# Optimization experiments

Measured on AMD Instinct MI355X. Metric: run time of the kernel, lower is better.

The kernel has to match this reference:

```python
import jax, jax.numpy as jnp
import numpy as np

# Irreps config: node = 64x0e + 32x1o, edge sh = 1x0e + 1x1o
N, E = 50000, 800000
MUL0, MUL1 = 64, 32
D_IN = MUL0 + 3 * MUL1          # 160
FC_H = 64
W_NUMEL = MUL0 + MUL0 + MUL1 + MUL1  # 192, per-instruction uvu weights
SQRT3 = 1.7320508075688772
ACT_C = 1.6791   # e3nn normalize2mom constant for silu


def setup_inputs() -> dict:
    key = jax.random.key(0)
    ks = jax.random.split(key, 11)
    return {
        "x": jax.random.normal(ks[0], (N, D_IN), jnp.float32),
        "edge_scalars": jax.random.uniform(ks[1], (E, FC_H), dtype=jnp.float32),
        "edge_attr_sh": jax.random.normal(ks[2], (E, 4), jnp.float32),
        "edge_index": jax.random.randint(ks[3], (2, E), 0, N),
        "w_fc1": jax.random.normal(ks[4], (FC_H, FC_H), jnp.float32),
        "w_fc2": jax.random.normal(ks[5], (FC_H, W_NUMEL), jnp.float32),
        "w_sc_s": jax.random.normal(ks[6], (MUL0, MUL0), jnp.float32),
        "w_sc_v": jax.random.normal(ks[7], (MUL1, MUL1), jnp.float32),
        "w_lin_s": jax.random.normal(ks[8], (96, MUL0), jnp.float32),
        "w_lin_v": jax.random.normal(ks[9], (96, MUL1), jnp.float32),
        "w_alpha": jax.random.normal(ks[10], (96, 1), jnp.float32) * 0.1,
    }


def reference(x, edge_scalars, edge_attr_sh, edge_index, w_fc1, w_fc2,
              w_sc_s, w_sc_v, w_lin_s, w_lin_v, w_alpha):
    src, dst = edge_index[0], edge_index[1]

    # --- fc: FullyConnectedNet([64, 64, 192], silu), e3nn fan-in norm ---
    h = jax.nn.silu(edge_scalars @ w_fc1 / np.sqrt(FC_H)) * ACT_C
    weight = h @ w_fc2 / np.sqrt(FC_H)                       # [E, 192]
    w0 = weight[:, :MUL0]                 # 0e x 0e -> 0e (mul 64)
    w1 = weight[:, MUL0:2 * MUL0]         # 0e x 1o -> 1o (mul 64)
    w2 = weight[:, 2 * MUL0:2 * MUL0 + MUL1]   # 1o x 0e -> 1o (mul 32)
    w3 = weight[:, 2 * MUL0 + MUL1:]           # 1o x 1o -> 0e (mul 32)

    # --- self connection: o3.Linear(in -> out), per-irrep mixing ---
    x_s = x[:, :MUL0]                                   # [N, 64]
    x_v = x[:, MUL0:].reshape(N, MUL1, 3)               # [N, 32, 3]
    sc_s = x_s @ w_sc_s / np.sqrt(MUL0)
    sc_v = jnp.einsum('nui,uw->nwi', x_v, w_sc_v) / np.sqrt(MUL1)
    sc_out = jnp.concatenate([sc_s, sc_v.reshape(N, 3 * MUL1)], axis=1)

    # --- gather + edge-weighted uvu tensor product ---
    gx_s = x_s[src]                                     # [E, 64]
    gx_v = x_v[src]                                     # [E, 32, 3]
    sh_s = edge_attr_sh[:, 0:1]                         # [E, 1]
    sh_v = edge_attr_sh[:, 1:4]                         # [E, 3]

    # path weights fold with w3j so factors cancel for 1o outputs
    mid_s0 = w0 * gx_s * sh_s                                        # [E,64] 0e
    mid_s1 = w3 * jnp.einsum('eui,ei->eu', gx_v, sh_v) / SQRT3       # [E,32] 0e
    mid_v0 = w1[:, :, None] * gx_s[:, :, None] * sh_v[:, None, :]    # [E,64,3] 1o
    mid_v1 = w2[:, :, None] * gx_v * sh_s[:, :, None]                # [E,32,3] 1o
    edge_feat = jnp.concatenate(
        [mid_s0, mid_s1, mid_v0.reshape(E, 3 * MUL0), mid_v1.reshape(E, 3 * MUL1)],
        axis=1)                                                      # [E, 384]

    # --- scatter-mean to destination nodes ---
    seg = jax.ops.segment_sum(edge_feat, dst, num_segments=N)
    cnt = jax.ops.segment_sum(jnp.ones((E,), edge_feat.dtype), dst, num_segments=N)
    mean = seg / jnp.maximum(cnt, 1.0)[:, None]                      # [N, 384]

    m_s = mean[:, :96]                                   # 96x0e
    m_v = mean[:, 96:].reshape(N, 96, 3)                 # 96x1o

    # --- alpha gate (o3.Linear mid -> 0e) and output linear ---
    alpha = m_s @ w_alpha / np.sqrt(96)                  # [N, 1]
    lin_s = m_s @ w_lin_s / np.sqrt(96)                  # [N, 64]
    lin_v = jnp.einsum('nui,uw->nwi', m_v, w_lin_v) / np.sqrt(96)
    lin_out = jnp.concatenate([lin_s, lin_v.reshape(N, 3 * MUL1)], axis=1)

    # sc.output_mask is all-ones here (every output irrep reachable)
    return sc_out + alpha * lin_out
```

## Files before the change

kernel.cpp:

```cpp
#include <hip/hip_runtime.h>
#include <hip/hip_bf16.h>

#define N_NODES 50000
#define N_EDGES 800000
#define MUL0 64
#define MUL1 32
#define D_IN 160
#define FC_H 64
#define W_NUMEL 192
#define FEAT 384
#define ACT_C 1.6791f
#define INV_SQRT3 0.57735026918962576f
#define RSQRT32 0.17677669529663687f
#define RSQRT96 0.10206207261596575f

#define TILE 64

typedef __attribute__((ext_vector_type(8))) short s16x8;
typedef __attribute__((ext_vector_type(4))) float f32x4;
typedef _Float16 h8 __attribute__((ext_vector_type(8)));
typedef __fp16 fp16x2 __attribute__((ext_vector_type(2)));

static __device__ __forceinline__ unsigned short f2bf(float f) {
    __hip_bfloat16 b = __float2bfloat16(f);
    return __builtin_bit_cast(unsigned short, b);
}

static __device__ __forceinline__ int swz(int row, int byte_in_row) {
    int unit = ((row & 1) << 2) | (byte_in_row >> 4);
    int su = unit ^ ((row >> 1) & 7);
    return (row >> 1) * 128 + su * 16 + (byte_in_row & 15);
}
static __device__ __forceinline__ h8 rdh8(const unsigned char* base, int row, int eb) {
    return *(const h8*)(base + swz(row, eb));
}


__global__ __launch_bounds__(256) void hist_kernel(const int* __restrict__ eidx,
                                                   int* __restrict__ cnt) {
    int e = blockIdx.x * 256 + threadIdx.x;
    if (e < N_EDGES) atomicAdd(&cnt[eidx[N_EDGES + e]], 1);
}

#define SCAN_NB 64
#define SCAN_CH ((N_NODES + SCAN_NB - 1) / SCAN_NB)

__global__ __launch_bounds__(256) void scanA_kernel(const int* __restrict__ cnt,
                                                    int* __restrict__ bsum) {
    __shared__ int sred[4];
    int b = blockIdx.x, t = threadIdx.x;
    int lim = min((b + 1) * SCAN_CH, N_NODES);
    int s = 0;
    for (int i = b * SCAN_CH + t; i < lim; i += 256) s += cnt[i];
    for (int d = 1; d < 64; d <<= 1) s += __shfl_xor(s, d);
    if ((t & 63) == 0) sred[t >> 6] = s;
    __syncthreads();
    if (t == 0) bsum[b] = sred[0] + sred[1] + sred[2] + sred[3];
}

__global__ __launch_bounds__(64) void scanB_kernel(const int* __restrict__ bsum,
                                                   int* __restrict__ boff) {
    int t = threadIdx.x;
    int v = bsum[t];
    int p = v;
    for (int d = 1; d < 64; d <<= 1) { int u = __shfl_up(p, d); if (t >= d) p += u; }
    boff[t] = p - v;
}

__global__ __launch_bounds__(256) void scanC_kernel(const int* __restrict__ cnt,
                                                    const int* __restrict__ boff,
                                                    int* __restrict__ fill) {
    __shared__ int s_w[4];
    int b = blockIdx.x, t = threadIdx.x;
    const int CH2 = (SCAN_CH + 255) / 256;
    int base = b * SCAN_CH + t * CH2;
    int lim = min((b + 1) * SCAN_CH, N_NODES);
    int s = 0;
#pragma unroll
    for (int k = 0; k < CH2; ++k) { int i = base + k; if (i < lim) s += cnt[i]; }
    int v = s;
    for (int d = 1; d < 64; d <<= 1) { int u = __shfl_up(v, d); if ((t & 63) >= d) v += u; }
    if ((t & 63) == 63) s_w[t >> 6] = v;
    __syncthreads();
    if (t == 0) { int run = 0; for (int w = 0; w < 4; ++w) { int tv = s_w[w]; s_w[w] = run; run += tv; } }
    __syncthreads();
    int run = boff[b] + s_w[t >> 6] + (v - s);
#pragma unroll
    for (int k = 0; k < CH2; ++k) {
        int i = base + k;
        if (i < lim) { fill[i] = run; run += cnt[i]; }
    }
}

__global__ __launch_bounds__(256) void scatter_ids_kernel(const int* __restrict__ eidx,
                                                          int* __restrict__ fill,
                                                          int* __restrict__ sorted_eid) {
    int e = blockIdx.x * 256 + threadIdx.x;
    if (e < N_EDGES) {
        int p = atomicAdd(&fill[eidx[N_EDGES + e]], 1);
        sorted_eid[p] = e;
    }
}

__global__ __launch_bounds__(256) void prep_w_kernel(
    const float* __restrict__ w_fc1,
    const float* __restrict__ w_fc2,
    const float* __restrict__ w_sc_s,
    const float* __restrict__ w_sc_v,
    const float* __restrict__ w_lin_s,
    const float* __restrict__ w_lin_v,
    unsigned short* __restrict__ w1t,
    unsigned short* __restrict__ w2t,
    unsigned short* __restrict__ wscs_t,
    unsigned short* __restrict__ wscv_t,
    unsigned short* __restrict__ wlins_t,
    unsigned short* __restrict__ wlinv_t)
{
    int i = blockIdx.x * 256 + threadIdx.x;
    if (i < 64 * 64)  w1t[i]    = f2bf(w_fc1[(i & 63) * FC_H + (i >> 6)]);
    if (i < 192 * 64) w2t[i]    = f2bf(w_fc2[(i & 63) * W_NUMEL + (i >> 6)]);
    if (i < 64 * 64)  wscs_t[i] = f2bf(w_sc_s[(i & 63) * 64 + (i >> 6)]);
    if (i < 32 * 32)  wscv_t[i] = f2bf(w_sc_v[(i & 31) * 32 + (i >> 5)]);
    if (i < 64 * 96)  wlins_t[i] = f2bf(w_lin_s[(i % 96) * 64 + (i / 96)]);
    if (i < 32 * 96)  wlinv_t[i] = f2bf(w_lin_v[(i % 96) * 32 + (i / 96)]);
}

#define X_OFF    0
#define W_OFF    20480
#define SH_OFF   45056
#define SID_OFF  45568
#define SEGN_OFF 45696
#define NSEG_OFF 45952
#define SMEM_SZ  45968

static __device__ __forceinline__ h8 seg_mask(const unsigned* vv, unsigned tgt) {
    h8 a;
#pragma unroll
    for (int w2 = 0; w2 < 4; ++w2) {
        a[w2 * 2]     = ((vv[w2] & 0xffffu) == tgt) ? (_Float16)1.f : (_Float16)0.f;
        a[w2 * 2 + 1] = ((vv[w2] >> 16)     == tgt) ? (_Float16)1.f : (_Float16)0.f;
    }
    return a;
}

__global__ __launch_bounds__(256) void edge_kernel(
    const float* __restrict__ x,
    const float* __restrict__ es,
    const float* __restrict__ sh,
    const int*   __restrict__ eidx,
    const int*   __restrict__ sorted_eid,
    const unsigned short* __restrict__ w1t,
    const unsigned short* __restrict__ w2t,
    float* __restrict__ accg)
{
    __shared__ __align__(16) unsigned char smem[SMEM_SZ];
    int* s_segnode = (int*)(smem + SEGN_OFF);
    unsigned short* s_sid = (unsigned short*)(smem + SID_OFF);

    const int t = threadIdx.x;
    const int l = t & 63;
    const int wv = t >> 6;
    const int lr = l & 15;
    const int lk = l >> 4;
    const int tile0 = blockIdx.x * TILE;

    int eid_own = sorted_eid[tile0 + wv * 16 + lr];
    float4 esf[4];
    {
        const float4* ep = (const float4*)(es + (size_t)eid_own * FC_H);
        esf[0] = ep[lk * 2];     esf[1] = ep[lk * 2 + 1];
        esf[2] = ep[8 + lk * 2]; esf[3] = ep[8 + lk * 2 + 1];
    }
    const int hs   = t >> 7;
    const int tt_h = t & 127;
    const int xe   = tt_h & 31;
    const int cgrp = tt_h >> 5;
    float4 xg[10];
    {
        const float4* xp = (const float4*)(x + (size_t)eidx[sorted_eid[tile0 + hs * 32 + xe]] * D_IN);
#pragma unroll
        for (int k = 0; k < 10; ++k) xg[k] = xp[cgrp * 10 + k];
    }
    float shv = sh[(size_t)sorted_eid[tile0 + (t >> 2)] * 4 + (t & 3)];
    if (wv == 0) {
        int dl = eidx[N_EDGES + sorted_eid[tile0 + l]];
        int nd = __shfl_down(dl, 1);
        bool flag = (l == 63) || (dl != nd);
        unsigned long long m = __ballot(flag);
        int sid = __popcll(m & ((1ull << l) - 1ull));
        s_sid[l] = (unsigned short)sid;
        if (flag) s_segnode[sid] = dl;
        if (l == 63) *(int*)(smem + NSEG_OFF) = sid + 1;
    }

    unsigned short* s_h = (unsigned short*)(smem + X_OFF);
    s16x8 afrag[2];
    {
        s16x8 a;
        a[0] = f2bf(esf[0].x); a[1] = f2bf(esf[0].y); a[2] = f2bf(esf[0].z); a[3] = f2bf(esf[0].w);
        a[4] = f2bf(esf[1].x); a[5] = f2bf(esf[1].y); a[6] = f2bf(esf[1].z); a[7] = f2bf(esf[1].w);
        afrag[0] = a;
        a[0] = f2bf(esf[2].x); a[1] = f2bf(esf[2].y); a[2] = f2bf(esf[2].z); a[3] = f2bf(esf[2].w);
        a[4] = f2bf(esf[3].x); a[5] = f2bf(esf[3].y); a[6] = f2bf(esf[3].z); a[7] = f2bf(esf[3].w);
        afrag[1] = a;
    }
#pragma unroll
    for (int nt = 0; nt < 4; ++nt) {
        f32x4 hacc = {0.f, 0.f, 0.f, 0.f};
#pragma unroll
        for (int kk = 0; kk < 2; ++kk) {
            s16x8 b = *(const s16x8*)(w1t + (nt * 16 + lr) * 64 + kk * 32 + lk * 8);
            hacc = __builtin_amdgcn_mfma_f32_16x16x32_bf16(afrag[kk], b, hacc, 0, 0, 0);
        }
#pragma unroll
        for (int q = 0; q < 4; ++q) {
            float aa = hacc[q] * 0.125f;
            float hv = aa * (1.f / (1.f + __expf(-aa))) * ACT_C;
            s_h[(wv * 16 + lk * 4 + q) * 72 + nt * 16 + lr] = f2bf(hv);
        }
    }
    s16x8 hfrag[2];
#pragma unroll
    for (int kk = 0; kk < 2; ++kk)
        hfrag[kk] = *(const s16x8*)(s_h + (wv * 16 + lr) * 72 + kk * 32 + lk * 8);
    __syncthreads();

    {
        const int ws = wv >> 1;
        const int ebyte = (wv & 1) * 32 + lk * 8;
        unsigned char* bw = smem + W_OFF + ws * 12288;
#pragma unroll
        for (int nt = 0; nt < 12; ++nt) {
            f32x4 acc = {0.f, 0.f, 0.f, 0.f};
#pragma unroll
            for (int kk = 0; kk < 2; ++kk) {
                s16x8 b = *(const s16x8*)(w2t + (nt * 16 + lr) * 64 + kk * 32 + lk * 8);
                acc = __builtin_amdgcn_mfma_f32_16x16x32_bf16(hfrag[kk], b, acc, 0, 0, 0);
            }
            int f = nt * 16 + lr;
            fp16x2 p0 = __builtin_amdgcn_cvt_pkrtz(acc[0] * 0.125f, acc[1] * 0.125f);
            fp16x2 p1 = __builtin_amdgcn_cvt_pkrtz(acc[2] * 0.125f, acc[3] * 0.125f);
            uint2 wval = { __builtin_bit_cast(unsigned, p0), __builtin_bit_cast(unsigned, p1) };
            *(uint2*)(bw + swz(f, ebyte)) = wval;
        }
    }
    {
        unsigned char* bx = smem + X_OFF + hs * 10240;
#pragma unroll
        for (int k = 0; k < 10; ++k) {
            float4 v = xg[k];
#pragma unroll
            for (int jj = 0; jj < 4; ++jj) {
                int r = (cgrp * 10 + k) * 4 + jj;
                float fv = (jj == 0) ? v.x : (jj == 1) ? v.y : (jj == 2) ? v.z : v.w;
                *(_Float16*)(bx + swz(r, xe * 2)) = (_Float16)fv;
            }
        }
    }
    {
        int e = t >> 2, c = t & 3;
        *(_Float16*)(smem + SH_OFF + (e >> 5) * 256 + swz(c, (e & 31) * 2)) = (_Float16)shv;
    }
    __syncthreads();

    const int nseg = *(const int*)(smem + NSEG_OFF);
    const int eb = lk * 16;

    h8 shreg[4][2];
    unsigned vv[2][4];
#pragma unroll
    for (int ks = 0; ks < 2; ++ks) {
#pragma unroll
        for (int r = 0; r < 4; ++r)
            shreg[r][ks] = rdh8(smem + SH_OFF + ks * 256, r, eb);
        uint4 sv = *(const uint4*)(smem + SID_OFF + ks * 64 + lk * 16);
        vv[ks][0] = sv.x; vv[ks][1] = sv.y; vv[ks][2] = sv.z; vv[ks][3] = sv.w;
    }

    h8 Bv[4][2];
    int fcol[4];
    bool cls3j[4] = {false, false, false, false};
#pragma unroll
    for (int ks = 0; ks < 2; ++ks) {
        const unsigned char* bx = smem + X_OFF + ks * 10240;
        const unsigned char* bw = smem + W_OFF + ks * 12288;
        if (wv == 0) {
#pragma unroll
            for (int jj = 0; jj < 4; ++jj) {
                int col = jj * 16 + lr;
                Bv[jj][ks] = rdh8(bw, col, eb) * rdh8(bx, col, eb);
                fcol[jj] = col;
            }
        } else if (wv == 1) {
#pragma unroll
            for (int jj = 0; jj < 4; ++jj) {
                int col = jj * 16 + lr;
                Bv[jj][ks] = rdh8(bw, 128 + col / 3, eb) * rdh8(bx, 64 + col, eb);
                fcol[jj] = 288 + col;
            }
        } else if (wv == 2) {
#pragma unroll
            for (int jj = 0; jj < 2; ++jj) {
                int col = 64 + jj * 16 + lr;
                Bv[jj][ks] = rdh8(bw, 128 + col / 3, eb) * rdh8(bx, 64 + col, eb);
                fcol[jj] = 288 + col;
            }
#pragma unroll
            for (int jj = 2; jj < 4; ++jj) {
                int col = (jj - 2) * 16 + lr;
                h8 d = rdh8(bx, 64 + 3 * col, eb)     * shreg[1][ks]
                     + rdh8(bx, 64 + 3 * col + 1, eb) * shreg[2][ks]
                     + rdh8(bx, 64 + 3 * col + 2, eb) * shreg[3][ks];
                Bv[jj][ks] = rdh8(bw, 160 + col, eb) * d;
                fcol[jj] = 64 + col;
                cls3j[jj] = true;
            }
        } else {
#pragma unroll
            for (int jj = 0; jj < 4; ++jj) {
                int col = jj * 16 + lr;
                Bv[jj][ks] = rdh8(bw, 64 + col, eb) * rdh8(bx, col, eb);
                fcol[jj] = 96 + 3 * col;
            }
        }
    }

    if (wv != 3) {
        const int npass = (nseg + 15) >> 4;
        for (int p = 0; p < npass; ++p) {
            h8 bm0 = seg_mask(vv[0], (unsigned)(p * 16 + lr));
            h8 bm1 = seg_mask(vv[1], (unsigned)(p * 16 + lr));
            h8 As0 = bm0 * shreg[0][0];
            h8 As1 = bm1 * shreg[0][1];
            const int m0 = p * 16 + lk * 4;
            float* nptr[4]; bool valid[4], atq[4];
#pragma unroll
            for (int q = 0; q < 4; ++q) {
                int sg = m0 + q;
                valid[q] = sg < nseg;
                int node = valid[q] ? s_segnode[sg] : 0;
                nptr[q] = accg + (size_t)node * FEAT;
                atq[q] = (sg == 0) || (sg == nseg - 1);
            }
#pragma unroll
            for (int jj = 0; jj < 4; ++jj) {
                f32x4 acc = {0.f, 0.f, 0.f, 0.f};
                acc = __builtin_amdgcn_mfma_f32_16x16x32_f16(cls3j[jj] ? bm0 : As0, Bv[jj][0], acc, 0, 0, 0);
                acc = __builtin_amdgcn_mfma_f32_16x16x32_f16(cls3j[jj] ? bm1 : As1, Bv[jj][1], acc, 0, 0, 0);
                const float sc = cls3j[jj] ? INV_SQRT3 : 1.f;
#pragma unroll
                for (int q = 0; q < 4; ++q) {
                    if (valid[q]) {
                        float v = acc[q] * sc;
                        float* a = nptr[q] + fcol[jj];
                        if (atq[q]) atomicAdd(a, v); else *a = v;
                    }
                }
            }
        }
    } else {
        const int npass = (3 * nseg + 15) >> 4;
        for (int p = 0; p < npass; ++p) {
            int m = p * 16 + lr;
            int sgA = m / 3, i3A = m - 3 * sgA;
            h8 mk0 = seg_mask(vv[0], (unsigned)sgA);
            h8 mk1 = seg_mask(vv[1], (unsigned)sgA);
            h8 A0 = mk0 * ((i3A == 0) ? shreg[1][0] : (i3A == 1) ? shreg[2][0] : shreg[3][0]);
            h8 A1 = mk1 * ((i3A == 0) ? shreg[1][1] : (i3A == 1) ? shreg[2][1] : shreg[3][1]);
            int m0 = p * 16 + lk * 4;
            int sgq = m0 / 3, rq = m0 - 3 * sgq;
            float* nptr[4]; int i3q[4]; bool valid[4], atq[4];
#pragma unroll
            for (int q = 0; q < 4; ++q) {
                valid[q] = sgq < nseg;
                int node = valid[q] ? s_segnode[sgq] : 0;
                nptr[q] = accg + (size_t)node * FEAT;
                i3q[q] = rq;
                atq[q] = (sgq == 0) || (sgq == nseg - 1);
                if (++rq == 3) { rq = 0; ++sgq; }
            }
#pragma unroll
            for (int jj = 0; jj < 4; ++jj) {
                f32x4 acc = {0.f, 0.f, 0.f, 0.f};
                acc = __builtin_amdgcn_mfma_f32_16x16x32_f16(A0, Bv[jj][0], acc, 0, 0, 0);
                acc = __builtin_amdgcn_mfma_f32_16x16x32_f16(A1, Bv[jj][1], acc, 0, 0, 0);
#pragma unroll
                for (int q = 0; q < 4; ++q) {
                    if (valid[q]) {
                        float* a = nptr[q] + fcol[jj] + i3q[q];
                        if (atq[q]) atomicAdd(a, acc[q]); else *a = acc[q];
                    }
                }
            }
        }
    }
}


static __device__ __forceinline__ s16x8 frag_c8(const float* p, float s) {
    float4 u = *(const float4*)p, v = *(const float4*)(p + 4);
    s16x8 a;
    a[0] = f2bf(u.x * s); a[1] = f2bf(u.y * s); a[2] = f2bf(u.z * s); a[3] = f2bf(u.w * s);
    a[4] = f2bf(v.x * s); a[5] = f2bf(v.y * s); a[6] = f2bf(v.z * s); a[7] = f2bf(v.w * s);
    return a;
}

__global__ __launch_bounds__(256) void node_kernel(
    const float* __restrict__ x,
    const float* __restrict__ accg,
    const int*   __restrict__ cnt,
    const unsigned short* __restrict__ wscs_t,
    const unsigned short* __restrict__ wscv_t,
    const unsigned short* __restrict__ wlins_t,
    const unsigned short* __restrict__ wlinv_t,
    const float* __restrict__ w_alpha,
    float* __restrict__ out)
{
    const int t = threadIdx.x;
    const int wv = t >> 6, l = t & 63;
    const int lr = l & 15, lk = l >> 4;
    const int n_base = blockIdx.x * 64 + wv * 16;
    const int nrow = n_base + lr;
    const int nclamp = min(nrow, N_NODES - 1);

    const float* mrow = accg + (size_t)nclamp * FEAT;
    const float* xrow = x + (size_t)nclamp * D_IN;
    const float rinv = 1.f / (float)max(cnt[nclamp], 1);

    s16x8 ax[2], ams[3], axv[3], amv[3][3];
#pragma unroll
    for (int kk = 0; kk < 2; ++kk) ax[kk] = frag_c8(xrow + kk * 32 + lk * 8, 1.f);
#pragma unroll
    for (int kk = 0; kk < 3; ++kk) ams[kk] = frag_c8(mrow + kk * 32 + lk * 8, rinv);
    {
        float xb[24];
        const float4* p = (const float4*)(xrow + 64 + 24 * lk);
#pragma unroll
        for (int q = 0; q < 6; ++q) ((float4*)xb)[q] = p[q];
#pragma unroll
        for (int i = 0; i < 3; ++i) {
            s16x8 a;
#pragma unroll
            for (int j = 0; j < 8; ++j) a[j] = f2bf(xb[3 * j + i]);
            axv[i] = a;
        }
    }
#pragma unroll
    for (int kk = 0; kk < 3; ++kk) {
        float mb[24];
        const float4* p = (const float4*)(mrow + 96 + 96 * kk + 24 * lk);
#pragma unroll
        for (int q = 0; q < 6; ++q) ((float4*)mb)[q] = p[q];
#pragma unroll
        for (int i = 0; i < 3; ++i) {
            s16x8 a;
#pragma unroll
            for (int j = 0; j < 8; ++j) a[j] = f2bf(mb[3 * j + i] * rinv);
            amv[i][kk] = a;
        }
    }

    float ap = 0.f;
    {
        float ab[24];
        const float4* p = (const float4*)(mrow + 24 * lk);
#pragma unroll
        for (int q = 0; q < 6; ++q) ((float4*)ab)[q] = p[q];
#pragma unroll
        for (int j = 0; j < 24; ++j) ap += ab[j] * rinv * w_alpha[lk * 24 + j];
    }
    ap += __shfl_xor(ap, 16);
    ap += __shfl_xor(ap, 32);
    const float alphav = ap * RSQRT96;

    f32x4 accA[4], accL[4];
#pragma unroll
    for (int nt = 0; nt < 4; ++nt) { accA[nt] = (f32x4){0,0,0,0}; accL[nt] = (f32x4){0,0,0,0}; }
#pragma unroll
    for (int nt = 0; nt < 4; ++nt) {
#pragma unroll
        for (int kk = 0; kk < 2; ++kk) {
            s16x8 b = *(const s16x8*)(wscs_t + (nt * 16 + lr) * 64 + kk * 32 + lk * 8);
            accA[nt] = __builtin_amdgcn_mfma_f32_16x16x32_bf16(ax[kk], b, accA[nt], 0, 0, 0);
        }
#pragma unroll
        for (int kk = 0; kk < 3; ++kk) {
            s16x8 b = *(const s16x8*)(wlins_t + (nt * 16 + lr) * 96 + kk * 32 + lk * 8);
            accL[nt] = __builtin_amdgcn_mfma_f32_16x16x32_bf16(ams[kk], b, accL[nt], 0, 0, 0);
        }
    }
    f32x4 accVs[3][2], accVl[3][2];
#pragma unroll
    for (int i = 0; i < 3; ++i)
#pragma unroll
        for (int nt = 0; nt < 2; ++nt) { accVs[i][nt] = (f32x4){0,0,0,0}; accVl[i][nt] = (f32x4){0,0,0,0}; }
#pragma unroll
    for (int i = 0; i < 3; ++i) {
#pragma unroll
        for (int nt = 0; nt < 2; ++nt) {
            s16x8 b = *(const s16x8*)(wscv_t + (nt * 16 + lr) * 32 + lk * 8);
            accVs[i][nt] = __builtin_amdgcn_mfma_f32_16x16x32_bf16(axv[i], b, accVs[i][nt], 0, 0, 0);
#pragma unroll
            for (int kk = 0; kk < 3; ++kk) {
                s16x8 b2 = *(const s16x8*)(wlinv_t + (nt * 16 + lr) * 96 + kk * 32 + lk * 8);
                accVl[i][nt] = __builtin_amdgcn_mfma_f32_16x16x32_bf16(amv[i][kk], b2, accVl[i][nt], 0, 0, 0);
            }
        }
    }

#pragma unroll
    for (int q = 0; q < 4; ++q) {
        int row = lk * 4 + q;
        float ar = __shfl(alphav, row);
        int n = n_base + row;
        bool ok = (n < N_NODES);
        float* orow = out + (size_t)n * 160;
#pragma unroll
        for (int nt = 0; nt < 4; ++nt) {
            float vout = accA[nt][q] * 0.125f + ar * accL[nt][q] * RSQRT96;
            if (ok) orow[nt * 16 + lr] = vout;
        }
#pragma unroll
        for (int i = 0; i < 3; ++i)
#pragma unroll
            for (int nt = 0; nt < 2; ++nt) {
                float vout = accVs[i][nt][q] * RSQRT32 + ar * accVl[i][nt][q] * RSQRT96;
                if (ok) orow[64 + 3 * (nt * 16 + lr) + i] = vout;
            }
    }
}


extern "C" void kernel_launch(void* const* d_in, const int* in_sizes, int n_in,
                              void* d_out, int out_size, void* d_ws, size_t ws_size,
                              hipStream_t stream) {
    const float* x        = (const float*)d_in[0];
    const float* es       = (const float*)d_in[1];
    const float* sh       = (const float*)d_in[2];
    const int*   eidx     = (const int*)d_in[3];
    const float* w_fc1    = (const float*)d_in[4];
    const float* w_fc2    = (const float*)d_in[5];
    const float* w_sc_s   = (const float*)d_in[6];
    const float* w_sc_v   = (const float*)d_in[7];
    const float* w_lin_s  = (const float*)d_in[8];
    const float* w_lin_v  = (const float*)d_in[9];
    const float* w_alpha  = (const float*)d_in[10];
    float* out = (float*)d_out;

    float* accg       = (float*)d_ws;
    int*   cnt        = (int*)(accg + (size_t)N_NODES * FEAT);
    int*   fill       = cnt + N_NODES;
    int*   sorted_eid = fill + N_NODES;
    unsigned short* w1t     = (unsigned short*)(sorted_eid + N_EDGES);
    unsigned short* w2t     = w1t + 64 * 64;
    unsigned short* wscs_t  = w2t + 192 * 64;
    unsigned short* wscv_t  = wscs_t + 64 * 64;
    unsigned short* wlins_t = wscv_t + 32 * 32;
    unsigned short* wlinv_t = wlins_t + 64 * 96;
    int* bsum = (int*)(wlinv_t + 32 * 96);
    int* boff = bsum + SCAN_NB;

    (void)hipMemsetAsync(d_ws, 0, ((size_t)N_NODES * FEAT + N_NODES) * 4, stream);
    hipLaunchKernelGGL(hist_kernel, dim3((N_EDGES + 255) / 256), dim3(256), 0, stream,
                       eidx, cnt);
    hipLaunchKernelGGL(scanA_kernel, dim3(SCAN_NB), dim3(256), 0, stream, cnt, bsum);
    hipLaunchKernelGGL(scanB_kernel, dim3(1), dim3(64), 0, stream, bsum, boff);
    hipLaunchKernelGGL(scanC_kernel, dim3(SCAN_NB), dim3(256), 0, stream, cnt, boff, fill);
    hipLaunchKernelGGL(scatter_ids_kernel, dim3((N_EDGES + 255) / 256), dim3(256), 0, stream,
                       eidx, fill, sorted_eid);
    hipLaunchKernelGGL(prep_w_kernel, dim3(48), dim3(256), 0, stream,
                       w_fc1, w_fc2, w_sc_s, w_sc_v, w_lin_s, w_lin_v,
                       w1t, w2t, wscs_t, wscv_t, wlins_t, wlinv_t);
    hipLaunchKernelGGL(edge_kernel, dim3(N_EDGES / TILE), dim3(256), 0, stream,
                       x, es, sh, eidx, sorted_eid, w1t, w2t, accg);
    hipLaunchKernelGGL(node_kernel, dim3((N_NODES + 63) / 64), dim3(256), 0, stream,
                       x, accg, cnt, wscs_t, wscv_t, wlins_t, wlinv_t, w_alpha, out);
}
```

Baseline: 453.6 us.

## Fuse preprocessing kernels, presort src/dst indices, and remap edge blocks across XCDs

Merges the histogram and weight-prep launches into one kernel and folds the single-block scan into scanC, which removes two kernel launches. The scatter step now also writes sorted source and destination arrays, so the edge kernel no longer does a double indirection through edge_index. The edge kernel remaps blockIdx so that consecutive tiles land on the same XCD, aiming for better L2 locality on the sorted destinations. The cost is extra global writes of two 800k-int arrays and a redundant 64-wide scan in every scanC block.

```diff
diff --git a/kernel.cpp b/kernel.cpp
--- a/kernel.cpp
+++ b/kernel.cpp
@@ -15,6 +15,7 @@
 #define RSQRT96 0.10206207261596575f
 
 #define TILE 64
+#define NWG_EDGE (N_EDGES / TILE)
 
 typedef __attribute__((ext_vector_type(8))) short s16x8;
 typedef __attribute__((ext_vector_type(4))) float f32x4;
@@ -36,73 +37,11 @@
 }
 
 
-__global__ __launch_bounds__(256) void hist_kernel(const int* __restrict__ eidx,
-                                                   int* __restrict__ cnt) {
-    int e = blockIdx.x * 256 + threadIdx.x;
-    if (e < N_EDGES) atomicAdd(&cnt[eidx[N_EDGES + e]], 1);
-}
-
-#define SCAN_NB 64
-#define SCAN_CH ((N_NODES + SCAN_NB - 1) / SCAN_NB)
-
-__global__ __launch_bounds__(256) void scanA_kernel(const int* __restrict__ cnt,
-                                                    int* __restrict__ bsum) {
-    __shared__ int sred[4];
-    int b = blockIdx.x, t = threadIdx.x;
-    int lim = min((b + 1) * SCAN_CH, N_NODES);
-    int s = 0;
-    for (int i = b * SCAN_CH + t; i < lim; i += 256) s += cnt[i];
-    for (int d = 1; d < 64; d <<= 1) s += __shfl_xor(s, d);
-    if ((t & 63) == 0) sred[t >> 6] = s;
-    __syncthreads();
-    if (t == 0) bsum[b] = sred[0] + sred[1] + sred[2] + sred[3];
-}
-
-__global__ __launch_bounds__(64) void scanB_kernel(const int* __restrict__ bsum,
-                                                   int* __restrict__ boff) {
-    int t = threadIdx.x;
-    int v = bsum[t];
-    int p = v;
-    for (int d = 1; d < 64; d <<= 1) { int u = __shfl_up(p, d); if (t >= d) p += u; }
-    boff[t] = p - v;
-}
-
-__global__ __launch_bounds__(256) void scanC_kernel(const int* __restrict__ cnt,
-                                                    const int* __restrict__ boff,
-                                                    int* __restrict__ fill) {
-    __shared__ int s_w[4];
-    int b = blockIdx.x, t = threadIdx.x;
-    const int CH2 = (SCAN_CH + 255) / 256;
-    int base = b * SCAN_CH + t * CH2;
-    int lim = min((b + 1) * SCAN_CH, N_NODES);
-    int s = 0;
-#pragma unroll
-    for (int k = 0; k < CH2; ++k) { int i = base + k; if (i < lim) s += cnt[i]; }
-    int v = s;
-    for (int d = 1; d < 64; d <<= 1) { int u = __shfl_up(v, d); if ((t & 63) >= d) v += u; }
-    if ((t & 63) == 63) s_w[t >> 6] = v;
-    __syncthreads();
-    if (t == 0) { int run = 0; for (int w = 0; w < 4; ++w) { int tv = s_w[w]; s_w[w] = run; run += tv; } }
-    __syncthreads();
-    int run = boff[b] + s_w[t >> 6] + (v - s);
-#pragma unroll
-    for (int k = 0; k < CH2; ++k) {
-        int i = base + k;
-        if (i < lim) { fill[i] = run; run += cnt[i]; }
-    }
-}
-
-__global__ __launch_bounds__(256) void scatter_ids_kernel(const int* __restrict__ eidx,
-                                                          int* __restrict__ fill,
-                                                          int* __restrict__ sorted_eid) {
-    int e = blockIdx.x * 256 + threadIdx.x;
-    if (e < N_EDGES) {
-        int p = atomicAdd(&fill[eidx[N_EDGES + e]], 1);
-        sorted_eid[p] = e;
-    }
-}
-
-__global__ __launch_bounds__(256) void prep_w_kernel(
+#define HIST_NB ((N_EDGES + 255) / 256)
+
+__global__ __launch_bounds__(256) void hist_prep_kernel(
+    const int*   __restrict__ eidx,
+    int*         __restrict__ cnt,
     const float* __restrict__ w_fc1,
     const float* __restrict__ w_fc2,
     const float* __restrict__ w_sc_s,
@@ -116,13 +55,83 @@
     unsigned short* __restrict__ wlins_t,
     unsigned short* __restrict__ wlinv_t)
 {
-    int i = blockIdx.x * 256 + threadIdx.x;
-    if (i < 64 * 64)  w1t[i]    = f2bf(w_fc1[(i & 63) * FC_H + (i >> 6)]);
-    if (i < 192 * 64) w2t[i]    = f2bf(w_fc2[(i & 63) * W_NUMEL + (i >> 6)]);
-    if (i < 64 * 64)  wscs_t[i] = f2bf(w_sc_s[(i & 63) * 64 + (i >> 6)]);
-    if (i < 32 * 32)  wscv_t[i] = f2bf(w_sc_v[(i & 31) * 32 + (i >> 5)]);
-    if (i < 64 * 96)  wlins_t[i] = f2bf(w_lin_s[(i % 96) * 64 + (i / 96)]);
-    if (i < 32 * 96)  wlinv_t[i] = f2bf(w_lin_v[(i % 96) * 32 + (i / 96)]);
+    int b = blockIdx.x;
+    if (b < HIST_NB) {
+        int e = b * 256 + threadIdx.x;
+        if (e < N_EDGES) atomicAdd(&cnt[eidx[N_EDGES + e]], 1);
+    } else {
+        int i = (b - HIST_NB) * 256 + threadIdx.x;
+        if (i < 64 * 64)  w1t[i]    = f2bf(w_fc1[(i & 63) * FC_H + (i >> 6)]);
+        if (i < 192 * 64) w2t[i]    = f2bf(w_fc2[(i & 63) * W_NUMEL + (i >> 6)]);
+        if (i < 64 * 64)  wscs_t[i] = f2bf(w_sc_s[(i & 63) * 64 + (i >> 6)]);
+        if (i < 32 * 32)  wscv_t[i] = f2bf(w_sc_v[(i & 31) * 32 + (i >> 5)]);
+        if (i < 64 * 96)  wlins_t[i] = f2bf(w_lin_s[(i % 96) * 64 + (i / 96)]);
+        if (i < 32 * 96)  wlinv_t[i] = f2bf(w_lin_v[(i % 96) * 32 + (i / 96)]);
+    }
+}
+
+#define SCAN_NB 64
+#define SCAN_CH ((N_NODES + SCAN_NB - 1) / SCAN_NB)
+
+__global__ __launch_bounds__(256) void scanA_kernel(const int* __restrict__ cnt,
+                                                    int* __restrict__ bsum) {
+    __shared__ int sred[4];
+    int b = blockIdx.x, t = threadIdx.x;
+    int lim = min((b + 1) * SCAN_CH, N_NODES);
+    int s = 0;
+    for (int i = b * SCAN_CH + t; i < lim; i += 256) s += cnt[i];
+    for (int d = 1; d < 64; d <<= 1) s += __shfl_xor(s, d);
+    if ((t & 63) == 0) sred[t >> 6] = s;
+    __syncthreads();
+    if (t == 0) bsum[b] = sred[0] + sred[1] + sred[2] + sred[3];
+}
+
+__global__ __launch_bounds__(256) void scanC_kernel(const int* __restrict__ cnt,
+                                                    const int* __restrict__ bsum,
+                                                    int* __restrict__ fill) {
+    __shared__ int s_w[4];
+    __shared__ int s_boff;
+    int b = blockIdx.x, t = threadIdx.x;
+    if (t < 64) {
+        int v = bsum[t];
+        int p = v;
+        for (int d = 1; d < 64; d <<= 1) { int u = __shfl_up(p, d); if (t >= d) p += u; }
+        if (t == b) s_boff = p - v;
+    }
+    const int CH2 = (SCAN_CH + 255) / 256;
+    int base = b * SCAN_CH + t * CH2;
+    int lim = min((b + 1) * SCAN_CH, N_NODES);
+    int s = 0;
+#pragma unroll
+    for (int k = 0; k < CH2; ++k) { int i = base + k; if (i < lim) s += cnt[i]; }
+    int v = s;
+    for (int d = 1; d < 64; d <<= 1) { int u = __shfl_up(v, d); if ((t & 63) >= d) v += u; }
+    if ((t & 63) == 63) s_w[t >> 6] = v;
+    __syncthreads();
+    if (t == 0) { int run = 0; for (int w = 0; w < 4; ++w) { int tv = s_w[w]; s_w[w] = run; run += tv; } }
+    __syncthreads();
+    int run = s_boff + s_w[t >> 6] + (v - s);
+#pragma unroll
+    for (int k = 0; k < CH2; ++k) {
+        int i = base + k;
+        if (i < lim) { fill[i] = run; run += cnt[i]; }
+    }
+}
+
+__global__ __launch_bounds__(256) void scatter_ids_kernel(const int* __restrict__ eidx,
+                                                          int* __restrict__ fill,
+                                                          int* __restrict__ sorted_eid,
+                                                          int* __restrict__ sorted_src,
+                                                          int* __restrict__ sorted_dst) {
+    int e = blockIdx.x * 256 + threadIdx.x;
+    if (e < N_EDGES) {
+        int d = eidx[N_EDGES + e];
+        int s = eidx[e];
+        int p = atomicAdd(&fill[d], 1);
+        sorted_eid[p] = e;
+        sorted_src[p] = s;
+        sorted_dst[p] = d;
+    }
 }
 
 #define X_OFF    0
@@ -147,8 +156,9 @@
     const float* __restrict__ x,
     const float* __restrict__ es,
     const float* __restrict__ sh,
-    const int*   __restrict__ eidx,
     const int*   __restrict__ sorted_eid,
+    const int*   __restrict__ sorted_src,
+    const int*   __restrict__ sorted_dst,
     const unsigned short* __restrict__ w1t,
     const unsigned short* __restrict__ w2t,
     float* __restrict__ accg)
@@ -162,7 +172,15 @@
     const int wv = t >> 6;
     const int lr = l & 15;
     const int lk = l >> 4;
-    const int tile0 = blockIdx.x * TILE;
+    int bid;
+    {
+        const int nwg = NWG_EDGE;
+        int orig = blockIdx.x;
+        int xcd = orig & 7, idx = orig >> 3;
+        int q = nwg >> 3, r = nwg & 7;
+        bid = (xcd < r ? xcd * (q + 1) : r * (q + 1) + (xcd - r) * q) + idx;
+    }
+    const int tile0 = bid * TILE;
 
     int eid_own = sorted_eid[tile0 + wv * 16 + lr];
     float4 esf[4];
@@ -177,13 +195,13 @@
     const int cgrp = tt_h >> 5;
     float4 xg[10];
     {
-        const float4* xp = (const float4*)(x + (size_t)eidx[sorted_eid[tile0 + hs * 32 + xe]] * D_IN);
+        const float4* xp = (const float4*)(x + (size_t)sorted_src[tile0 + hs * 32 + xe] * D_IN);
 #pragma unroll
         for (int k = 0; k < 10; ++k) xg[k] = xp[cgrp * 10 + k];
     }
     float shv = sh[(size_t)sorted_eid[tile0 + (t >> 2)] * 4 + (t & 3)];
     if (wv == 0) {
-        int dl = eidx[N_EDGES + sorted_eid[tile0 + l]];
+        int dl = sorted_dst[tile0 + l];
         int nd = __shfl_down(dl, 1);
         bool flag = (l == 63) || (dl != nd);
         unsigned long long m = __ballot(flag);
@@ -551,28 +569,26 @@
     int*   cnt        = (int*)(accg + (size_t)N_NODES * FEAT);
     int*   fill       = cnt + N_NODES;
     int*   sorted_eid = fill + N_NODES;
-    unsigned short* w1t     = (unsigned short*)(sorted_eid + N_EDGES);
+    int*   sorted_src = sorted_eid + N_EDGES;
+    int*   sorted_dst = sorted_src + N_EDGES;
+    unsigned short* w1t     = (unsigned short*)(sorted_dst + N_EDGES);
     unsigned short* w2t     = w1t + 64 * 64;
     unsigned short* wscs_t  = w2t + 192 * 64;
     unsigned short* wscv_t  = wscs_t + 64 * 64;
     unsigned short* wlins_t = wscv_t + 32 * 32;
     unsigned short* wlinv_t = wlins_t + 64 * 96;
     int* bsum = (int*)(wlinv_t + 32 * 96);
-    int* boff = bsum + SCAN_NB;
 
     (void)hipMemsetAsync(d_ws, 0, ((size_t)N_NODES * FEAT + N_NODES) * 4, stream);
-    hipLaunchKernelGGL(hist_kernel, dim3((N_EDGES + 255) / 256), dim3(256), 0, stream,
-                       eidx, cnt);
+    hipLaunchKernelGGL(hist_prep_kernel, dim3(HIST_NB + 48), dim3(256), 0, stream,
+                       eidx, cnt, w_fc1, w_fc2, w_sc_s, w_sc_v, w_lin_s, w_lin_v,
+                       w1t, w2t, wscs_t, wscv_t, wlins_t, wlinv_t);
     hipLaunchKernelGGL(scanA_kernel, dim3(SCAN_NB), dim3(256), 0, stream, cnt, bsum);
-    hipLaunchKernelGGL(scanB_kernel, dim3(1), dim3(64), 0, stream, bsum, boff);
-    hipLaunchKernelGGL(scanC_kernel, dim3(SCAN_NB), dim3(256), 0, stream, cnt, boff, fill);
+    hipLaunchKernelGGL(scanC_kernel, dim3(SCAN_NB), dim3(256), 0, stream, cnt, bsum, fill);
     hipLaunchKernelGGL(scatter_ids_kernel, dim3((N_EDGES + 255) / 256), dim3(256), 0, stream,
-                       eidx, fill, sorted_eid);
-    hipLaunchKernelGGL(prep_w_kernel, dim3(48), dim3(256), 0, stream,
-                       w_fc1, w_fc2, w_sc_s, w_sc_v, w_lin_s, w_lin_v,
-                       w1t, w2t, wscs_t, wscv_t, wlins_t, wlinv_t);
-    hipLaunchKernelGGL(edge_kernel, dim3(N_EDGES / TILE), dim3(256), 0, stream,
-                       x, es, sh, eidx, sorted_eid, w1t, w2t, accg);
+                       eidx, fill, sorted_eid, sorted_src, sorted_dst);
+    hipLaunchKernelGGL(edge_kernel, dim3(NWG_EDGE), dim3(256), 0, stream,
+                       x, es, sh, sorted_eid, sorted_src, sorted_dst, w1t, w2t, accg);
     hipLaunchKernelGGL(node_kernel, dim3((N_NODES + 63) / 64), dim3(256), 0, stream,
                        x, accg, cnt, wscs_t, wscv_t, wlins_t, wlinv_t, w_alpha, out);
 }
```

Measured after the change: 453.5 us. About the same (-0.0%).
